# Kernel optimization log

Measured on AMD Instinct MI355X. Metric: run time of the kernel, lower is better.

The kernel has to match this reference:

```python
import jax, jax.numpy as jnp
import numpy as np
import math

B, S, D = 4, 2048, 1024
H = 16
DH = D // H
NEG = -1e20


def setup_inputs() -> dict:
    key = jax.random.key(0)
    ks = jax.random.split(key, 8)
    Q_batch = jax.random.normal(ks[0], (B, S, D), dtype=jnp.float32)
    K_batch = jax.random.normal(ks[1], (B, S, D), dtype=jnp.float32)
    V_batch = jax.random.normal(ks[2], (B, S, D), dtype=jnp.float32)
    valid_lens = jax.random.randint(ks[3], (B,), 0, S).astype(jnp.int64)
    # LazyLinear weights, stored as (in, out) so projection is x @ W
    sc = 1.0 / math.sqrt(D)
    Wq = jax.random.normal(ks[4], (D, D), dtype=jnp.float32) * sc
    Wk = jax.random.normal(ks[5], (D, D), dtype=jnp.float32) * sc
    Wv = jax.random.normal(ks[6], (D, D), dtype=jnp.float32) * sc
    Wo = jax.random.normal(ks[7], (D, D), dtype=jnp.float32) * sc
    return {"Q_batch": Q_batch, "K_batch": K_batch, "V_batch": V_batch,
            "valid_lens": valid_lens, "Wq": Wq, "Wk": Wk, "Wv": Wv, "Wo": Wo}


def reference(Q_batch, K_batch, V_batch, valid_lens, Wq, Wk, Wv, Wo):
    b, nq, _ = Q_batch.shape
    nk = K_batch.shape[1]
    # project and split heads (feature dim split head-major, matching transpose_qkv)
    q = (Q_batch @ Wq).reshape(b, nq, H, DH).transpose(0, 2, 1, 3)  # (b,h,nq,dh)
    k = (K_batch @ Wk).reshape(b, nk, H, DH).transpose(0, 2, 1, 3)  # (b,h,nk,dh)
    v = (V_batch @ Wv).reshape(b, nk, H, DH).transpose(0, 2, 1, 3)  # (b,h,nk,dh)
    scores = jnp.einsum('bhqd,bhkd->bhqk', q, k) / math.sqrt(DH)
    # mask keys at position >= valid_lens[b] (shared across heads and queries)
    key_pos = jnp.arange(nk)
    mask = key_pos[None, None, None, :] < valid_lens[:, None, None, None]
    scores = jnp.where(mask, scores, NEG)
    w = jax.nn.softmax(scores, axis=-1)  # dropout rate 0 -> identity
    o = jnp.einsum('bhqk,bhkd->bhqd', w, v)           # (b,h,nq,dh)
    o = o.transpose(0, 2, 1, 3).reshape(b, nq, H * DH)  # concat heads
    return o @ Wo
```

## Files before the change

kernel.cpp:

```cpp
#include <hip/hip_runtime.h>
#include <stdint.h>

typedef unsigned short u16;
using bf16x8 = __attribute__((ext_vector_type(8))) __bf16;
using f32x4  = __attribute__((ext_vector_type(4))) float;
using u16x8  = __attribute__((ext_vector_type(8))) unsigned short;
using u16x4  = __attribute__((ext_vector_type(4))) unsigned short;

#define NH   16
#define DHD  64
#define SEQ  2048
#define DD   1024

__device__ inline u16 bfbits(float f) {
    __bf16 h = (__bf16)f;
    return __builtin_bit_cast(u16, h);
}

__device__ inline void gld16(const u16* g, u16* l) {
    __builtin_amdgcn_global_load_lds(
        (const __attribute__((address_space(1))) void*)g,
        (__attribute__((address_space(3))) void*)l,
        16, 0, 0);
}

__global__ __launch_bounds__(256) void transpose4(
    const float* __restrict__ s0, const float* __restrict__ s1,
    const float* __restrict__ s2, const float* __restrict__ s3,
    u16* __restrict__ d0, u16* __restrict__ d1,
    u16* __restrict__ d2, u16* __restrict__ d3)
{
    const float* src = s0; u16* dst = d0;
    if (blockIdx.z == 1) { src = s1; dst = d1; }
    else if (blockIdx.z == 2) { src = s2; dst = d2; }
    else if (blockIdx.z == 3) { src = s3; dst = d3; }

    __shared__ u16 tile[32][33];
    int tx = threadIdx.x, ty = threadIdx.y;
    int x = blockIdx.x * 32 + tx;
    int y0 = blockIdx.y * 32 + ty;
#pragma unroll
    for (int i = 0; i < 32; i += 8)
        tile[ty + i][tx] = bfbits(src[(size_t)(y0 + i) * DD + x]);
    __syncthreads();
    int x2 = blockIdx.y * 32 + tx;
    int y2 = blockIdx.x * 32 + ty;
#pragma unroll
    for (int i = 0; i < 32; i += 8)
        dst[(size_t)(y2 + i) * DD + x2] = tile[tx][ty + i];
}

__global__ __launch_bounds__(256) void cvt3(
    const float* __restrict__ s0, const float* __restrict__ s1,
    const float* __restrict__ s2,
    u16* __restrict__ d0, u16* __restrict__ d1, u16* __restrict__ d2)
{
    const float* src = s0; u16* dst = d0;
    if (blockIdx.z == 1) { src = s1; dst = d1; }
    else if (blockIdx.z == 2) { src = s2; dst = d2; }
    size_t i = ((size_t)blockIdx.x * 256 + threadIdx.x) * 8;
    f32x4 a = *(const f32x4*)&src[i];
    f32x4 b = *(const f32x4*)&src[i + 4];
    u16x8 o;
#pragma unroll
    for (int j = 0; j < 4; ++j) { o[j] = bfbits(a[j]); o[j + 4] = bfbits(b[j]); }
    *(u16x8*)&dst[i] = o;
}

__global__ __launch_bounds__(256) void cvt1(
    const float* __restrict__ src, u16* __restrict__ dst)
{
    size_t i = ((size_t)blockIdx.x * 256 + threadIdx.x) * 8;
    f32x4 a = *(const f32x4*)&src[i];
    f32x4 b = *(const f32x4*)&src[i + 4];
    u16x8 o;
#pragma unroll
    for (int j = 0; j < 4; ++j) { o[j] = bfbits(a[j]); o[j + 4] = bfbits(b[j]); }
    *(u16x8*)&dst[i] = o;
}

template<int MODE>
__global__ __launch_bounds__(256) void gemm_bt16(
    const u16* __restrict__ A0, const u16* __restrict__ A1, const u16* __restrict__ A2,
    const u16* __restrict__ B0, const u16* __restrict__ B1, const u16* __restrict__ B2,
    void* __restrict__ C0, void* __restrict__ C1, void* __restrict__ C2)
{
    const int K = 1024;
    const u16* A = A0; const u16* Bt = B0; void* C = C0;
    if (MODE == 3) {
        if (blockIdx.z == 1) { A = A1; Bt = B1; C = C1; }
        else if (blockIdx.z == 2) { A = A2; Bt = B2; C = C2; }
    }

    __shared__ __align__(16) u16 As[2][128 * 32];
    __shared__ __align__(16) u16 Bs[2][128 * 32];

    const int t = threadIdx.x;
    const int wave = t >> 6, lane = t & 63;
    const int l15 = lane & 15, q4 = lane >> 4;
    const int wm = (wave >> 1) * 64, wn = (wave & 1) * 64;

    const int gx = gridDim.x;
    const int nwg = gx * gridDim.y;
    int flat = blockIdx.y * gx + blockIdx.x;
    flat = (flat & 7) * (nwg >> 3) + (flat >> 3);
    const int m0 = (flat / gx) * 128, n0 = (flat % gx) * 128;

    const int ar = t >> 2;
    const int ac = (t & 3) * 8;

    const u16* gA = &A [(size_t)(m0 + ar) * K + ac];
    const u16* gB = &Bt[(size_t)(n0 + ar) * K + ac];
    u16* lA0 = &As[0][t * 8];
    u16* lA1 = &As[1][t * 8];
    u16* lB0 = &Bs[0][t * 8];
    u16* lB1 = &Bs[1][t * 8];

    f32x4 acc[4][4] = {};

    for (int k0 = 0; k0 < K; k0 += 64) {
        __syncthreads();
        gld16(gA + k0,                   lA0);
        gld16(gA + (size_t)64 * K + k0,  lA0 + 64 * 32);
        gld16(gA + k0 + 32,              lA1);
        gld16(gA + (size_t)64 * K + k0 + 32, lA1 + 64 * 32);
        gld16(gB + k0,                   lB0);
        gld16(gB + (size_t)64 * K + k0,  lB0 + 64 * 32);
        gld16(gB + k0 + 32,              lB1);
        gld16(gB + (size_t)64 * K + k0 + 32, lB1 + 64 * 32);
        __syncthreads();

#pragma unroll
        for (int hf = 0; hf < 2; ++hf) {
            bf16x8 af[4], bfr[4];
#pragma unroll
            for (int i = 0; i < 4; ++i) {
                af[i]  = *(const bf16x8*)&As[hf][(wm + i * 16 + l15) * 32 + q4 * 8];
                bfr[i] = *(const bf16x8*)&Bs[hf][(wn + i * 16 + l15) * 32 + q4 * 8];
            }
#pragma unroll
            for (int i = 0; i < 4; ++i)
#pragma unroll
                for (int j = 0; j < 4; ++j)
                    acc[i][j] = __builtin_amdgcn_mfma_f32_16x16x32_bf16(af[i], bfr[j], acc[i][j], 0, 0, 0);
        }
    }

    const bool vt_store = (MODE == 2) || (MODE == 3 && blockIdx.z == 2);

#pragma unroll
    for (int i = 0; i < 4; ++i) {
        int row_l = wm + i * 16 + q4 * 4;
#pragma unroll
        for (int j = 0; j < 4; ++j) {
            int col = n0 + wn + j * 16 + l15;
            if (MODE == 1) {
#pragma unroll
                for (int r = 0; r < 4; ++r) {
                    int row = m0 + row_l + r;
                    ((float*)C)[(size_t)row * DD + col] = acc[i][j][r];
                }
            } else if (vt_store) {
                int row = m0 + row_l;
                int b = row >> 11, s = row & (SEQ - 1);
                int h = col >> 6, dh = col & (DHD - 1);
                u16x4 pk;
#pragma unroll
                for (int r = 0; r < 4; ++r) pk[r] = bfbits(acc[i][j][r]);
                *(u16x4*)&((u16*)C)[(((size_t)(b * NH + h) * DHD + dh) << 11) | s] = pk;
            } else {
#pragma unroll
                for (int r = 0; r < 4; ++r) {
                    int row = m0 + row_l + r;
                    int b = row >> 11, s = row & (SEQ - 1);
                    int h = col >> 6, dh = col & (DHD - 1);
                    ((u16*)C)[(((size_t)(b * NH + h) * SEQ + s) << 6) | dh] = bfbits(acc[i][j][r]);
                }
            }
        }
    }
}

__global__ __launch_bounds__(256, 4) void attn(
    const u16* __restrict__ q_ws, const u16* __restrict__ k_ws,
    const u16* __restrict__ vT_ws, const int* __restrict__ valid_lens,
    u16* __restrict__ o_ws)
{
    int flat = blockIdx.y * gridDim.x + blockIdx.x;
    flat = (flat & 7) * ((gridDim.x * gridDim.y) >> 3) + (flat >> 3);
    const int qt = flat % gridDim.x;
    const int bh = flat / gridDim.x;
    const int b = bh >> 4, h = bh & 15;
    const int valid = valid_lens[b];
    const bool valid0 = (valid == 0);
    const int valid_eff = valid0 ? SEQ : valid;
    const int kt_n = (valid_eff + 63) >> 6;
    const float c2 = valid0 ? 0.f : 0.18033688011112042f;
    const float M2 = 17.312340490667562f;

    __shared__ u16 Ks[64][72];
    __shared__ u16 Vt[64][72];
    __shared__ u16 Ps[4][32][72];

    const int t = threadIdx.x;
    const int wave = t >> 6, lane = t & 63;
    const int l15 = lane & 15, q4 = lane >> 4;

    const size_t base  = (size_t)bh * SEQ * DHD;
    const size_t vbase = (size_t)bh * DHD * SEQ;

    const int q0 = qt * 128 + wave * 32;

    u16x8 ou;
#pragma unroll
    for (int j = 0; j < 8; ++j) ou[j] = 0x3F80;
    const bf16x8 ones = __builtin_bit_cast(bf16x8, ou);

    bf16x8 qf[2][2];
#pragma unroll
    for (int mi = 0; mi < 2; ++mi)
#pragma unroll
        for (int c = 0; c < 2; ++c)
            qf[mi][c] = *(const bf16x8*)&q_ws[base + (size_t)(q0 + mi * 16 + l15) * DHD + c * 32 + q4 * 8];

    f32x4 o4[2][4] = {};
    f32x4 l_acc[2] = {};

    for (int kt = 0; kt < kt_n; ++kt) {
        __syncthreads();
#pragma unroll
        for (int p = 0; p < 2; ++p) {
            int r = p * 32 + (t >> 3), c = (t & 7) * 8;
            *(u16x8*)&Ks[r][c] = *(const u16x8*)&k_ws[base + (size_t)(kt * 64 + r) * DHD + c];
            *(u16x8*)&Vt[r][c] = *(const u16x8*)&vT_ws[vbase + (size_t)r * SEQ + kt * 64 + c];
        }
        __syncthreads();

        f32x4 s4[2][4] = {};
#pragma unroll
        for (int c = 0; c < 2; ++c)
#pragma unroll
            for (int ni = 0; ni < 4; ++ni) {
                bf16x8 kf = *(const bf16x8*)&Ks[ni * 16 + l15][c * 32 + q4 * 8];
#pragma unroll
                for (int mi = 0; mi < 2; ++mi)
                    s4[mi][ni] = __builtin_amdgcn_mfma_f32_16x16x32_bf16(kf, qf[mi][c], s4[mi][ni], 0, 0, 0);
            }

        const bool tile_full = valid0 || (kt * 64 + 64 <= valid_eff);
        if (tile_full) {
#pragma unroll
            for (int mi = 0; mi < 2; ++mi) {
                int qrow = mi * 16 + l15;
#pragma unroll
                for (int ni = 0; ni < 4; ++ni) {
                    u16x4 pk;
#pragma unroll
                    for (int r = 0; r < 4; ++r) {
                        float p = exp2f(__builtin_fmaf(s4[mi][ni][r], c2, -M2));
                        pk[r] = bfbits(p);
                    }
                    *(u16x4*)&Ps[wave][qrow][ni * 16 + q4 * 4] = pk;
                }
            }
        } else {
#pragma unroll
            for (int mi = 0; mi < 2; ++mi) {
                int qrow = mi * 16 + l15;
#pragma unroll
                for (int ni = 0; ni < 4; ++ni) {
                    u16x4 pk;
#pragma unroll
                    for (int r = 0; r < 4; ++r) {
                        bool ok = (kt * 64 + ni * 16 + q4 * 4 + r) < valid_eff;
                        float arg = ok ? __builtin_fmaf(s4[mi][ni][r], c2, -M2) : -1e30f;
                        pk[r] = bfbits(exp2f(arg));
                    }
                    *(u16x4*)&Ps[wave][qrow][ni * 16 + q4 * 4] = pk;
                }
            }
        }

#pragma unroll
        for (int c = 0; c < 2; ++c) {
            bf16x8 pf[2];
#pragma unroll
            for (int mi = 0; mi < 2; ++mi) {
                pf[mi] = *(const bf16x8*)&Ps[wave][mi * 16 + l15][c * 32 + q4 * 8];
                l_acc[mi] = __builtin_amdgcn_mfma_f32_16x16x32_bf16(pf[mi], ones, l_acc[mi], 0, 0, 0);
            }
#pragma unroll
            for (int dt = 0; dt < 4; ++dt) {
                bf16x8 vf = *(const bf16x8*)&Vt[dt * 16 + l15][c * 32 + q4 * 8];
#pragma unroll
                for (int mi = 0; mi < 2; ++mi)
                    o4[mi][dt] = __builtin_amdgcn_mfma_f32_16x16x32_bf16(pf[mi], vf, o4[mi][dt], 0, 0, 0);
            }
        }
    }

#pragma unroll
    for (int mi = 0; mi < 2; ++mi) {
        float inv[4];
#pragma unroll
        for (int r = 0; r < 4; ++r) inv[r] = 1.0f / l_acc[mi][r];
        int qrow = q0 + mi * 16 + q4 * 4;
#pragma unroll
        for (int dt = 0; dt < 4; ++dt) {
            int dh = dt * 16 + l15;
#pragma unroll
            for (int r = 0; r < 4; ++r) {
                float v = o4[mi][dt][r] * inv[r];
                o_ws[((size_t)(b * SEQ + qrow + r) << 10) | (h * DHD + dh)] = bfbits(v);
            }
        }
    }
}

extern "C" void kernel_launch(void* const* d_in, const int* in_sizes, int n_in,
                              void* d_out, int out_size, void* d_ws, size_t ws_size,
                              hipStream_t stream)
{
    (void)in_sizes; (void)n_in; (void)out_size;
    const float* Q  = (const float*)d_in[0];
    const float* Kb = (const float*)d_in[1];
    const float* V  = (const float*)d_in[2];
    const int*   vl = (const int*)d_in[3];
    const float* Wq = (const float*)d_in[4];
    const float* Wk = (const float*)d_in[5];
    const float* Wv = (const float*)d_in[6];
    const float* Wo = (const float*)d_in[7];
    float* out = (float*)d_out;

    char* ws = (char*)d_ws;
    u16* WqT   = (u16*)(ws + (size_t)0);
    u16* WkT   = (u16*)(ws + ((size_t)2 << 20));
    u16* WvT   = (u16*)(ws + ((size_t)4 << 20));
    u16* WoT   = (u16*)(ws + ((size_t)6 << 20));
    u16* q_ws  = (u16*)(ws + ((size_t)8 << 20));
    u16* k_ws  = (u16*)(ws + ((size_t)24 << 20));
    u16* vT_ws = (u16*)(ws + ((size_t)40 << 20));
    u16* o_ws  = (u16*)(ws + ((size_t)56 << 20));
    u16* Qbf   = (u16*)(ws + ((size_t)72 << 20));
    u16* Kbf   = (u16*)(ws + ((size_t)88 << 20));
    u16* Vbf   = (u16*)(ws + ((size_t)104 << 20));

    transpose4<<<dim3(32, 32, 4), dim3(32, 8), 0, stream>>>(
        Wq, Wk, Wv, Wo, WqT, WkT, WvT, WoT);

    const bool fused = ws_size >= ((size_t)120 << 20);
    if (fused) {
        cvt3<<<dim3(4096, 1, 3), 256, 0, stream>>>(Q, Kb, V, Qbf, Kbf, Vbf);
        gemm_bt16<3><<<dim3(8, 64, 3), 256, 0, stream>>>(
            Qbf, Kbf, Vbf, WqT, WkT, WvT, q_ws, k_ws, vT_ws);
    } else {
        cvt1<<<4096, 256, 0, stream>>>(Q, o_ws);
        gemm_bt16<0><<<dim3(8, 64), 256, 0, stream>>>(
            o_ws, nullptr, nullptr, WqT, nullptr, nullptr, q_ws, nullptr, nullptr);
        cvt1<<<4096, 256, 0, stream>>>(Kb, o_ws);
        gemm_bt16<0><<<dim3(8, 64), 256, 0, stream>>>(
            o_ws, nullptr, nullptr, WkT, nullptr, nullptr, k_ws, nullptr, nullptr);
        cvt1<<<4096, 256, 0, stream>>>(V, o_ws);
        gemm_bt16<2><<<dim3(8, 64), 256, 0, stream>>>(
            o_ws, nullptr, nullptr, WvT, nullptr, nullptr, vT_ws, nullptr, nullptr);
    }

    attn<<<dim3(16, 64), 256, 0, stream>>>(q_ws, k_ws, vT_ws, vl, o_ws);

    gemm_bt16<1><<<dim3(8, 64), 256, 0, stream>>>(
        o_ws, nullptr, nullptr, WoT, nullptr, nullptr, out, nullptr, nullptr);
}
```

Baseline: 334.0 us.

## Double-buffer K/V tiles via async global-to-LDS loads with XOR swizzle

```diff
diff --git a/kernel.cpp b/kernel.cpp
--- a/kernel.cpp
+++ b/kernel.cpp
@@ -181,16 +181,14 @@
     }
 }
 
-__global__ __launch_bounds__(256, 4) void attn(
+__global__ __launch_bounds__(256, 3) void attn(
     const u16* __restrict__ q_ws, const u16* __restrict__ k_ws,
     const u16* __restrict__ vT_ws, const int* __restrict__ valid_lens,
     u16* __restrict__ o_ws)
 {
-    int flat = blockIdx.y * gridDim.x + blockIdx.x;
-    flat = (flat & 7) * ((gridDim.x * gridDim.y) >> 3) + (flat >> 3);
-    const int qt = flat % gridDim.x;
-    const int bh = flat / gridDim.x;
+    const int bh = blockIdx.y;
     const int b = bh >> 4, h = bh & 15;
+    const int qt = blockIdx.x;
     const int valid = valid_lens[b];
     const bool valid0 = (valid == 0);
     const int valid_eff = valid0 ? SEQ : valid;
@@ -198,8 +196,7 @@
     const float c2 = valid0 ? 0.f : 0.18033688011112042f;
     const float M2 = 17.312340490667562f;
 
-    __shared__ u16 Ks[64][72];
-    __shared__ u16 Vt[64][72];
+    __shared__ __align__(16) u16 KV[2][2][64 * 64];
     __shared__ u16 Ps[4][32][72];
 
     const int t = threadIdx.x;
@@ -211,6 +208,12 @@
 
     const int q0 = qt * 128 + wave * 32;
 
+    const int sr0 = wave * 16 + (lane >> 3);
+    const int cg  = ((lane & 7) ^ (sr0 & 7)) * 8;
+    const u16* gK = &k_ws [base  + (size_t)sr0 * DHD + cg];
+    const u16* gV = &vT_ws[vbase + (size_t)sr0 * SEQ + cg];
+    const int ldst = sr0 * 64 + (lane & 7) * 8;
+
     u16x8 ou;
 #pragma unroll
     for (int j = 0; j < 8; ++j) ou[j] = 0x3F80;
@@ -226,22 +229,37 @@
     f32x4 o4[2][4] = {};
     f32x4 l_acc[2] = {};
 
+    const int swz = (l15 & 7) * 8;
+
+    {
+        gld16(gK,                 &KV[0][0][ldst]);
+        gld16(gK + 512,           &KV[0][0][ldst + 512]);
+        gld16(gV,                 &KV[0][1][ldst]);
+        gld16(gV + (size_t)8 * SEQ, &KV[0][1][ldst + 512]);
+    }
+
+    int cur = 0;
     for (int kt = 0; kt < kt_n; ++kt) {
         __syncthreads();
-#pragma unroll
-        for (int p = 0; p < 2; ++p) {
-            int r = p * 32 + (t >> 3), c = (t & 7) * 8;
-            *(u16x8*)&Ks[r][c] = *(const u16x8*)&k_ws[base + (size_t)(kt * 64 + r) * DHD + c];
-            *(u16x8*)&Vt[r][c] = *(const u16x8*)&vT_ws[vbase + (size_t)r * SEQ + kt * 64 + c];
-        }
-        __syncthreads();
+        if (kt + 1 < kt_n) {
+            const u16* kk = gK + (size_t)(kt + 1) * 64 * DHD;
+            const u16* vv = gV + (size_t)(kt + 1) * 64;
+            int bf = cur ^ 1;
+            gld16(kk,                 &KV[bf][0][ldst]);
+            gld16(kk + 512,           &KV[bf][0][ldst + 512]);
+            gld16(vv,                 &KV[bf][1][ldst]);
+            gld16(vv + (size_t)8 * SEQ, &KV[bf][1][ldst + 512]);
+        }
+
+        const u16* KK = KV[cur][0];
+        const u16* VV = KV[cur][1];
 
         f32x4 s4[2][4] = {};
 #pragma unroll
         for (int c = 0; c < 2; ++c)
 #pragma unroll
             for (int ni = 0; ni < 4; ++ni) {
-                bf16x8 kf = *(const bf16x8*)&Ks[ni * 16 + l15][c * 32 + q4 * 8];
+                bf16x8 kf = *(const bf16x8*)&KK[(ni * 16 + l15) * 64 + ((c * 32 + q4 * 8) ^ swz)];
 #pragma unroll
                 for (int mi = 0; mi < 2; ++mi)
                     s4[mi][ni] = __builtin_amdgcn_mfma_f32_16x16x32_bf16(kf, qf[mi][c], s4[mi][ni], 0, 0, 0);
@@ -291,12 +309,13 @@
             }
 #pragma unroll
             for (int dt = 0; dt < 4; ++dt) {
-                bf16x8 vf = *(const bf16x8*)&Vt[dt * 16 + l15][c * 32 + q4 * 8];
+                bf16x8 vf = *(const bf16x8*)&VV[(dt * 16 + l15) * 64 + ((c * 32 + q4 * 8) ^ swz)];
 #pragma unroll
                 for (int mi = 0; mi < 2; ++mi)
                     o4[mi][dt] = __builtin_amdgcn_mfma_f32_16x16x32_bf16(pf[mi], vf, o4[mi][dt], 0, 0, 0);
             }
         }
+        cur ^= 1;
     }
 
 #pragma unroll
```

New measurement: 313.5 us. 6.1% less time.
